# Optimization experiments

Hardware: AMD Instinct MI355X
Metric: run time of the kernel (lower is better)

## Reference

```python
import jax, jax.numpy as jnp
import numpy as np

N_NODES = 50000
N_EDGES = 600000
N_GRAPHS = 100
IN_DIM, HID, OUT = 128, 128, 64
K = 2  # DGL TAGConv default hop count


def setup_inputs() -> dict:
    key = jax.random.key(0)
    ks = jax.random.split(key, 8)
    x = jax.random.normal(ks[0], (N_NODES, IN_DIM), dtype=jnp.float32)
    src = jax.random.randint(ks[1], (N_EDGES,), 0, N_NODES)
    dst = jax.random.randint(ks[2], (N_EDGES,), 0, N_NODES)
    graph_id = jnp.sort(jax.random.randint(ks[3], (N_NODES,), 0, N_GRAPHS))
    # TAGConv lin: Linear(in_feats*(K+1), out_feats), stored as (in*(K+1), out)
    W1 = jax.random.normal(ks[4], (IN_DIM * (K + 1), HID), dtype=jnp.float32) / np.sqrt(IN_DIM * (K + 1))
    b1 = jnp.zeros((HID,), dtype=jnp.float32)
    W2 = jax.random.normal(ks[5], (HID * (K + 1), OUT), dtype=jnp.float32) / np.sqrt(HID * (K + 1))
    b2 = jnp.zeros((OUT,), dtype=jnp.float32)
    return {"x": x, "W1": W1, "b1": b1, "W2": W2, "b2": b2,
            "src": src, "dst": dst, "graph_id": graph_id}


def _tagconv(h, src, dst, norm, W, b):
    """DGL TAGConv: relu(concat_k (D^-1/2 A D^-1/2)^k h @ W + b), k=0..K."""
    feats = [h]
    cur = h
    for _ in range(K):
        cur = cur * norm[:, None]
        cur = jax.ops.segment_sum(cur[src], dst, num_segments=N_NODES)
        cur = cur * norm[:, None]
        feats.append(cur)
    out = jnp.concatenate(feats, axis=-1) @ W + b
    return jax.nn.relu(out)


def reference(x, W1, b1, W2, b2, src, dst, graph_id):
    # symmetric norm from in-degrees (clamped to 1), as in DGL TAGConv
    deg = jax.ops.segment_sum(jnp.ones_like(dst, dtype=x.dtype), dst, num_segments=N_NODES)
    norm = jnp.clip(deg, 1.0, None) ** -0.5
    h = _tagconv(x, src, dst, norm, W1, b1)
    h = _tagconv(h, src, dst, norm, W2, b2)
    # MaxPooling readout: per-graph max over nodes
    return jax.ops.segment_max(h, graph_id, num_segments=N_GRAPHS)
```

## Files before the change

### kernel.cpp

```cpp
#include <hip/hip_runtime.h>
#include <hip/hip_bf16.h>

#define N_NODES 50000
#define N_EDGES 600000
#define N_GRAPHS 100
#define M_PAD 50176

typedef __bf16 bf16_t;
typedef __attribute__((ext_vector_type(8))) __bf16 bf16x8;
typedef __attribute__((ext_vector_type(2))) __bf16 bf16x2;
typedef __attribute__((ext_vector_type(4))) float f32x4;

__global__ void degk(const int* __restrict__ dst, int* __restrict__ deg, int n) {
    int i = blockIdx.x * 256 + threadIdx.x;
    if (i < n) atomicAdd(&deg[dst[i]], 1);
}

__global__ void normk(const int* __restrict__ deg, float* __restrict__ norm, int n) {
    int i = blockIdx.x * 256 + threadIdx.x;
    if (i < n) {
        float d = fmaxf((float)deg[i], 1.0f);
        norm[i] = 1.0f / sqrtf(d);
    }
}

__global__ __launch_bounds__(1024) void scan1(const int* __restrict__ deg,
                                              int* __restrict__ row_off,
                                              int* __restrict__ partial, int n) {
    __shared__ int buf[1024];
    int i = blockIdx.x * 1024 + threadIdx.x;
    int v = (i < n) ? deg[i] : 0;
    buf[threadIdx.x] = v;
    __syncthreads();
    for (int off = 1; off < 1024; off <<= 1) {
        int t = (threadIdx.x >= off) ? buf[threadIdx.x - off] : 0;
        __syncthreads();
        buf[threadIdx.x] += t;
        __syncthreads();
    }
    if (i < n) row_off[i + 1] = buf[threadIdx.x];
    if (threadIdx.x == 1023) partial[blockIdx.x] = buf[1023];
}

__global__ void scan2(int* __restrict__ partial, int nchunks) {
    int lane = threadIdx.x;
    int v = (lane < nchunks) ? partial[lane] : 0;
    for (int off = 1; off < 64; off <<= 1) {
        int t = __shfl_up(v, off, 64);
        if (lane >= off) v += t;
    }
    int ex = __shfl_up(v, 1, 64);
    if (lane == 0) ex = 0;
    if (lane < nchunks) partial[lane] = ex;
}

__global__ void scan3(int* __restrict__ row_off, const int* __restrict__ partial, int n) {
    int i = blockIdx.x * 256 + threadIdx.x;
    if (i == 0) row_off[0] = 0;
    if (i < n) row_off[i + 1] += partial[i >> 10];
}

__global__ void scatterk(const int* __restrict__ src, const int* __restrict__ dst,
                         const int* __restrict__ row_off, int* __restrict__ cursor,
                         int* __restrict__ csr_src, int n) {
    int e = blockIdx.x * 256 + threadIdx.x;
    if (e >= n) return;
    int d = dst[e];
    int pos = atomicAdd(&cursor[d], 1);
    csr_src[row_off[d] + pos] = src[e];
}

__global__ void prescale(const float* __restrict__ x, const float* __restrict__ norm,
                         bf16_t* __restrict__ xb, bf16_t* __restrict__ xs, int n) {
    int i = blockIdx.x * 256 + threadIdx.x;
    if (i >= n * 64) return;
    int node = i >> 6;
    int c = (i & 63) * 2;
    float2 v = *(const float2*)(x + (size_t)node * 128 + c);
    float nd = norm[node];
    bf16x2 vb; vb[0] = (bf16_t)v.x; vb[1] = (bf16_t)v.y;
    bf16x2 vs; vs[0] = (bf16_t)(v.x * nd); vs[1] = (bf16_t)(v.y * nd);
    *(bf16x2*)(xb + (size_t)node * 128 + c) = vb;
    *(bf16x2*)(xs + (size_t)node * 128 + c) = vs;
}

__global__ void permW(const float* __restrict__ W, bf16_t* __restrict__ Wp, int K, int N) {
    int i = blockIdx.x * 256 + threadIdx.x;
    if (i >= K * N) return;
    int k = i / N, n = i - k * N;
    int kt = k >> 5, q = (k >> 3) & 3, j = k & 7;
    int nt = n >> 4, ln = n & 15;
    int lane = q * 16 + ln;
    Wp[(((size_t)kt * (N >> 4) + nt) * 64 + lane) * 8 + j] = (bf16_t)W[i];
}

template <bool SCALED>
__global__ __launch_bounds__(256) void spmm_bf16(const bf16_t* __restrict__ in,
                                                 bf16_t* __restrict__ out_c,
                                                 bf16_t* __restrict__ out_s,
                                                 const float* __restrict__ norm,
                                                 const int* __restrict__ row_off,
                                                 const int* __restrict__ csr_src, int n) {
    int tid = threadIdx.x;
    int sub = tid >> 4;
    int l   = tid & 15;
    int node = blockIdx.x * 16 + sub;
    if (node >= n) return;
    int e0 = row_off[node], e1 = row_off[node + 1];
    const bf16_t* col = in + l * 8;
    float acc[8] = {};
    int e = e0;
    for (; e + 4 <= e1; e += 4) {
        int s0 = csr_src[e + 0];
        int s1 = csr_src[e + 1];
        int s2 = csr_src[e + 2];
        int s3 = csr_src[e + 3];
        bf16x8 v0 = *(const bf16x8*)(col + (size_t)s0 * 128);
        bf16x8 v1 = *(const bf16x8*)(col + (size_t)s1 * 128);
        bf16x8 v2 = *(const bf16x8*)(col + (size_t)s2 * 128);
        bf16x8 v3 = *(const bf16x8*)(col + (size_t)s3 * 128);
#pragma unroll
        for (int j = 0; j < 8; j++)
            acc[j] += ((float)v0[j] + (float)v1[j]) + ((float)v2[j] + (float)v3[j]);
    }
    for (; e < e1; e++) {
        int s = csr_src[e];
        bf16x8 v = *(const bf16x8*)(col + (size_t)s * 128);
#pragma unroll
        for (int j = 0; j < 8; j++) acc[j] += (float)v[j];
    }
    float nd = norm[node];
    bf16x8 oc, os;
#pragma unroll
    for (int j = 0; j < 8; j++) {
        float c = acc[j] * nd;
        oc[j] = (bf16_t)c;
        os[j] = (bf16_t)(c * nd);
    }
    *(bf16x8*)(out_c + (size_t)node * 128 + l * 8) = oc;
    if (SCALED) *(bf16x8*)(out_s + (size_t)node * 128 + l * 8) = os;
}

template <int NT, bool LAYER1>
__global__ __launch_bounds__(256) void gemm_mfma(const bf16_t* __restrict__ f0,
                                                 const bf16_t* __restrict__ f1,
                                                 const bf16_t* __restrict__ f2,
                                                 const bf16_t* __restrict__ Wp,
                                                 const float* __restrict__ bias,
                                                 const float* __restrict__ norm,
                                                 bf16_t* __restrict__ out_b,
                                                 bf16_t* __restrict__ out_s,
                                                 float* __restrict__ out_f, int M) {
    int wave = threadIdx.x >> 6;
    int lane = threadIdx.x & 63;
    int q = lane >> 4, ln = lane & 15;
    int row0 = blockIdx.x * 128 + wave * 32;

    f32x4 acc[2][NT] = {};
    const bf16_t* feats[3] = {f0, f1, f2};
    const bf16x8* Wf = (const bf16x8*)Wp;

#pragma unroll
    for (int kc = 0; kc < 12; kc++) {
        const bf16_t* A = feats[kc >> 2] + (size_t)(kc & 3) * 32 + q * 8;
        bf16x8 a0 = *(const bf16x8*)(A + (size_t)(row0 + ln) * 128);
        bf16x8 a1 = *(const bf16x8*)(A + (size_t)(row0 + 16 + ln) * 128);
        const bf16x8* Bp = Wf + (size_t)kc * NT * 64 + lane;
#pragma unroll
        for (int nt = 0; nt < NT; nt++) {
            bf16x8 b = Bp[nt * 64];
            acc[0][nt] = __builtin_amdgcn_mfma_f32_16x16x32_bf16(a0, b, acc[0][nt], 0, 0, 0);
            acc[1][nt] = __builtin_amdgcn_mfma_f32_16x16x32_bf16(a1, b, acc[1][nt], 0, 0, 0);
        }
    }

    float bv[NT];
#pragma unroll
    for (int nt = 0; nt < NT; nt++) bv[nt] = bias[nt * 16 + ln];

#pragma unroll
    for (int mt = 0; mt < 2; mt++) {
#pragma unroll
        for (int r = 0; r < 4; r++) {
            int row = row0 + mt * 16 + q * 4 + r;
            if (row >= M) continue;
            float nd = LAYER1 ? norm[row] : 0.f;
#pragma unroll
            for (int nt = 0; nt < NT; nt++) {
                int col = nt * 16 + ln;
                float val = fmaxf(acc[mt][nt][r] + bv[nt], 0.f);
                if (LAYER1) {
                    out_b[(size_t)row * 128 + col] = (bf16_t)val;
                    out_s[(size_t)row * 128 + col] = (bf16_t)(val * nd);
                } else {
                    out_f[(size_t)row * 64 + col] = val;
                }
            }
        }
    }
}

__global__ __launch_bounds__(256) void maxpool2(const float* __restrict__ hF,
                                                const int* __restrict__ gid,
                                                unsigned int* __restrict__ out, int n) {
    int wave = threadIdx.x >> 6;
    int lane = threadIdx.x & 63;
    int n0 = blockIdx.x * 256 + wave * 64;
    if (n0 >= n) return;
    int n1 = min(n0 + 64, n);
    int cur = gid[n0];
    float m = 0.f;
    int i = n0;
    for (; i + 4 <= n1; i += 4) {
        int g0 = gid[i + 0], g1 = gid[i + 1], g2 = gid[i + 2], g3 = gid[i + 3];
        float v0 = hF[(size_t)(i + 0) * 64 + lane];
        float v1 = hF[(size_t)(i + 1) * 64 + lane];
        float v2 = hF[(size_t)(i + 2) * 64 + lane];
        float v3 = hF[(size_t)(i + 3) * 64 + lane];
        if (g0 != cur) { atomicMax(&out[cur * 64 + lane], __float_as_uint(m)); cur = g0; m = v0; } else m = fmaxf(m, v0);
        if (g1 != cur) { atomicMax(&out[cur * 64 + lane], __float_as_uint(m)); cur = g1; m = v1; } else m = fmaxf(m, v1);
        if (g2 != cur) { atomicMax(&out[cur * 64 + lane], __float_as_uint(m)); cur = g2; m = v2; } else m = fmaxf(m, v2);
        if (g3 != cur) { atomicMax(&out[cur * 64 + lane], __float_as_uint(m)); cur = g3; m = v3; } else m = fmaxf(m, v3);
    }
    for (; i < n1; i++) {
        int g = gid[i];
        float v = hF[(size_t)i * 64 + lane];
        if (g != cur) { atomicMax(&out[cur * 64 + lane], __float_as_uint(m)); cur = g; m = v; }
        else m = fmaxf(m, v);
    }
    atomicMax(&out[cur * 64 + lane], __float_as_uint(m));
}

extern "C" void kernel_launch(void* const* d_in, const int* in_sizes, int n_in,
                              void* d_out, int out_size, void* d_ws, size_t ws_size,
                              hipStream_t stream) {
    const float* x  = (const float*)d_in[0];
    const float* W1 = (const float*)d_in[1];
    const float* b1 = (const float*)d_in[2];
    const float* W2 = (const float*)d_in[3];
    const float* b2 = (const float*)d_in[4];
    const int* src  = (const int*)d_in[5];
    const int* dst  = (const int*)d_in[6];
    const int* gid  = (const int*)d_in[7];
    float* out = (float*)d_out;

    char* ws = (char*)d_ws;
    size_t off = 0;
    auto take = [&](size_t bytes) {
        void* p = ws + off;
        off = (off + bytes + 255) & ~(size_t)255;
        return p;
    };
    int* deg     = (int*)take((size_t)N_NODES * 4);
    int* cursor  = (int*)take((size_t)N_NODES * 4);
    size_t zero_bytes = off;
    float* norm  = (float*)take((size_t)N_NODES * 4);
    int* row_off = (int*)take((size_t)(N_NODES + 1) * 4);
    int* partial = (int*)take(64 * 4);
    int* csr_src = (int*)take((size_t)N_EDGES * 4);
    bf16_t* Wp1  = (bf16_t*)take((size_t)384 * 128 * 2);
    bf16_t* Wp2  = (bf16_t*)take((size_t)384 * 64 * 2);
    bf16_t* B0 = (bf16_t*)take((size_t)M_PAD * 128 * 2);
    bf16_t* B1 = (bf16_t*)take((size_t)M_PAD * 128 * 2);
    bf16_t* B2 = (bf16_t*)take((size_t)M_PAD * 128 * 2);
    bf16_t* B3 = (bf16_t*)take((size_t)M_PAD * 128 * 2);
    bf16_t* B4 = (bf16_t*)take((size_t)M_PAD * 128 * 2);
    bf16_t* B5 = (bf16_t*)take((size_t)M_PAD * 128 * 2);
    (void)ws_size; (void)in_sizes; (void)n_in; (void)out_size;

    hipMemsetAsync(d_ws, 0, zero_bytes, stream);
    hipMemsetAsync(d_out, 0, (size_t)N_GRAPHS * 64 * 4, stream);

    degk<<<(N_EDGES + 255) / 256, 256, 0, stream>>>(dst, deg, N_EDGES);
    normk<<<(N_NODES + 255) / 256, 256, 0, stream>>>(deg, norm, N_NODES);

    int nchunks = (N_NODES + 1023) / 1024;
    scan1<<<nchunks, 1024, 0, stream>>>(deg, row_off, partial, N_NODES);
    scan2<<<1, 64, 0, stream>>>(partial, nchunks);
    scan3<<<(N_NODES + 255) / 256, 256, 0, stream>>>(row_off, partial, N_NODES);
    scatterk<<<(N_EDGES + 255) / 256, 256, 0, stream>>>(src, dst, row_off, cursor, csr_src, N_EDGES);

    prescale<<<(N_NODES * 64 + 255) / 256, 256, 0, stream>>>(x, norm, B0, B1, N_NODES);
    permW<<<(384 * 128 + 255) / 256, 256, 0, stream>>>(W1, Wp1, 384, 128);
    permW<<<(384 * 64 + 255) / 256, 256, 0, stream>>>(W2, Wp2, 384, 64);

    int spmm_grid = (N_NODES + 15) / 16;
    int gemm_grid = M_PAD / 128;
    spmm_bf16<true><<<spmm_grid, 256, 0, stream>>>(B1, B2, B4, norm, row_off, csr_src, N_NODES);
    spmm_bf16<false><<<spmm_grid, 256, 0, stream>>>(B4, B3, nullptr, norm, row_off, csr_src, N_NODES);
    gemm_mfma<8, true><<<gemm_grid, 256, 0, stream>>>(B0, B2, B3, Wp1, b1, norm, B5, B1, nullptr, N_NODES);
    spmm_bf16<true><<<spmm_grid, 256, 0, stream>>>(B1, B2, B4, norm, row_off, csr_src, N_NODES);
    spmm_bf16<false><<<spmm_grid, 256, 0, stream>>>(B4, B3, nullptr, norm, row_off, csr_src, N_NODES);
    gemm_mfma<4, false><<<gemm_grid, 256, 0, stream>>>(B5, B2, B3, Wp2, b2, nullptr, nullptr, nullptr, (float*)B0, N_NODES);
    maxpool2<<<(N_NODES + 255) / 256, 256, 0, stream>>>((const float*)B0, gid, (unsigned int*)out, N_NODES);
}
```

Before: 308.8 us.

## Sort nodes by degree and process two nodes per SpMM thread group

Adds a counting sort of nodes by in-degree (histogram, scan, permutation) so neighbouring thread groups in the SpMM handle nodes with similar degree, which reduces wave divergence. Each 16-lane group now processes two nodes at once, interleaving their gathers so more loads are in flight. The cost is three extra small kernels, scattered output writes through the permutation, and higher register pressure from two accumulator sets.

```diff
diff --git a/kernel.cpp b/kernel.cpp
--- a/kernel.cpp
+++ b/kernel.cpp
@@ -70,6 +70,33 @@
     csr_src[row_off[d] + pos] = src[e];
 }
 
+__global__ void histk(const int* __restrict__ deg, int* __restrict__ hist, int n) {
+    int i = blockIdx.x * 256 + threadIdx.x;
+    if (i < n) atomicAdd(&hist[min(deg[i], 127)], 1);
+}
+
+__global__ void hscan(const int* __restrict__ hist, int* __restrict__ boff) {
+    __shared__ int b[128];
+    int t = threadIdx.x;
+    b[t] = hist[t];
+    __syncthreads();
+    if (t == 0) {
+        int s = 0;
+        for (int i = 0; i < 128; i++) { int v = b[i]; b[i] = s; s += v; }
+    }
+    __syncthreads();
+    boff[t] = b[t];
+}
+
+__global__ void permk(const int* __restrict__ deg, const int* __restrict__ boff,
+                      int* __restrict__ cur, int* __restrict__ perm, int n) {
+    int i = blockIdx.x * 256 + threadIdx.x;
+    if (i >= n) return;
+    int b = min(deg[i], 127);
+    int p = atomicAdd(&cur[b], 1);
+    perm[boff[b] + p] = i;
+}
+
 __global__ void prescale(const float* __restrict__ x, const float* __restrict__ norm,
                          bf16_t* __restrict__ xb, bf16_t* __restrict__ xs, int n) {
     int i = blockIdx.x * 256 + threadIdx.x;
@@ -100,45 +127,91 @@
                                                  bf16_t* __restrict__ out_s,
                                                  const float* __restrict__ norm,
                                                  const int* __restrict__ row_off,
-                                                 const int* __restrict__ csr_src, int n) {
+                                                 const int* __restrict__ csr_src,
+                                                 const int* __restrict__ perm, int n) {
     int tid = threadIdx.x;
     int sub = tid >> 4;
     int l   = tid & 15;
-    int node = blockIdx.x * 16 + sub;
-    if (node >= n) return;
-    int e0 = row_off[node], e1 = row_off[node + 1];
+    int base = blockIdx.x * 32 + sub * 2;
+    if (base >= n) return;
+    int nodeA = perm[base];
+    bool hasB = (base + 1 < n);
+    int nodeB = hasB ? perm[base + 1] : nodeA;
+
+    int a0 = row_off[nodeA], a1 = row_off[nodeA + 1];
+    int b0 = row_off[nodeB], b1 = row_off[nodeB + 1];
     const bf16_t* col = in + l * 8;
-    float acc[8] = {};
-    int e = e0;
-    for (; e + 4 <= e1; e += 4) {
-        int s0 = csr_src[e + 0];
-        int s1 = csr_src[e + 1];
-        int s2 = csr_src[e + 2];
-        int s3 = csr_src[e + 3];
+    float accA[8] = {}, accB[8] = {};
+
+    int da = a1 - a0, db = b1 - b0;
+    int c4 = (da < db ? da : db) & ~3;
+    int ea = a0, eb = b0;
+    for (int k = 0; k < c4; k += 4) {
+        int sA0 = csr_src[ea + 0], sA1 = csr_src[ea + 1], sA2 = csr_src[ea + 2], sA3 = csr_src[ea + 3];
+        int sB0 = csr_src[eb + 0], sB1 = csr_src[eb + 1], sB2 = csr_src[eb + 2], sB3 = csr_src[eb + 3];
+        bf16x8 vA0 = *(const bf16x8*)(col + (size_t)sA0 * 128);
+        bf16x8 vA1 = *(const bf16x8*)(col + (size_t)sA1 * 128);
+        bf16x8 vA2 = *(const bf16x8*)(col + (size_t)sA2 * 128);
+        bf16x8 vA3 = *(const bf16x8*)(col + (size_t)sA3 * 128);
+        bf16x8 vB0 = *(const bf16x8*)(col + (size_t)sB0 * 128);
+        bf16x8 vB1 = *(const bf16x8*)(col + (size_t)sB1 * 128);
+        bf16x8 vB2 = *(const bf16x8*)(col + (size_t)sB2 * 128);
+        bf16x8 vB3 = *(const bf16x8*)(col + (size_t)sB3 * 128);
+#pragma unroll
+        for (int j = 0; j < 8; j++) {
+            accA[j] += ((float)vA0[j] + (float)vA1[j]) + ((float)vA2[j] + (float)vA3[j]);
+            accB[j] += ((float)vB0[j] + (float)vB1[j]) + ((float)vB2[j] + (float)vB3[j]);
+        }
+        ea += 4; eb += 4;
+    }
+    for (; ea + 4 <= a1; ea += 4) {
+        int s0 = csr_src[ea + 0], s1 = csr_src[ea + 1], s2 = csr_src[ea + 2], s3 = csr_src[ea + 3];
         bf16x8 v0 = *(const bf16x8*)(col + (size_t)s0 * 128);
         bf16x8 v1 = *(const bf16x8*)(col + (size_t)s1 * 128);
         bf16x8 v2 = *(const bf16x8*)(col + (size_t)s2 * 128);
         bf16x8 v3 = *(const bf16x8*)(col + (size_t)s3 * 128);
 #pragma unroll
         for (int j = 0; j < 8; j++)
-            acc[j] += ((float)v0[j] + (float)v1[j]) + ((float)v2[j] + (float)v3[j]);
-    }
-    for (; e < e1; e++) {
-        int s = csr_src[e];
+            accA[j] += ((float)v0[j] + (float)v1[j]) + ((float)v2[j] + (float)v3[j]);
+    }
+    for (; ea < a1; ea++) {
+        int s = csr_src[ea];
         bf16x8 v = *(const bf16x8*)(col + (size_t)s * 128);
 #pragma unroll
-        for (int j = 0; j < 8; j++) acc[j] += (float)v[j];
-    }
-    float nd = norm[node];
-    bf16x8 oc, os;
+        for (int j = 0; j < 8; j++) accA[j] += (float)v[j];
+    }
+    for (; eb + 4 <= b1; eb += 4) {
+        int s0 = csr_src[eb + 0], s1 = csr_src[eb + 1], s2 = csr_src[eb + 2], s3 = csr_src[eb + 3];
+        bf16x8 v0 = *(const bf16x8*)(col + (size_t)s0 * 128);
+        bf16x8 v1 = *(const bf16x8*)(col + (size_t)s1 * 128);
+        bf16x8 v2 = *(const bf16x8*)(col + (size_t)s2 * 128);
+        bf16x8 v3 = *(const bf16x8*)(col + (size_t)s3 * 128);
+#pragma unroll
+        for (int j = 0; j < 8; j++)
+            accB[j] += ((float)v0[j] + (float)v1[j]) + ((float)v2[j] + (float)v3[j]);
+    }
+    for (; eb < b1; eb++) {
+        int s = csr_src[eb];
+        bf16x8 v = *(const bf16x8*)(col + (size_t)s * 128);
+#pragma unroll
+        for (int j = 0; j < 8; j++) accB[j] += (float)v[j];
+    }
+
+    float ndA = norm[nodeA], ndB = norm[nodeB];
+    bf16x8 ocA, osA, ocB, osB;
 #pragma unroll
     for (int j = 0; j < 8; j++) {
-        float c = acc[j] * nd;
-        oc[j] = (bf16_t)c;
-        os[j] = (bf16_t)(c * nd);
-    }
-    *(bf16x8*)(out_c + (size_t)node * 128 + l * 8) = oc;
-    if (SCALED) *(bf16x8*)(out_s + (size_t)node * 128 + l * 8) = os;
+        float cA = accA[j] * ndA;
+        ocA[j] = (bf16_t)cA; osA[j] = (bf16_t)(cA * ndA);
+        float cB = accB[j] * ndB;
+        ocB[j] = (bf16_t)cB; osB[j] = (bf16_t)(cB * ndB);
+    }
+    *(bf16x8*)(out_c + (size_t)nodeA * 128 + l * 8) = ocA;
+    if (SCALED) *(bf16x8*)(out_s + (size_t)nodeA * 128 + l * 8) = osA;
+    if (hasB) {
+        *(bf16x8*)(out_c + (size_t)nodeB * 128 + l * 8) = ocB;
+        if (SCALED) *(bf16x8*)(out_s + (size_t)nodeB * 128 + l * 8) = osB;
+    }
 }
 
 template <int NT, bool LAYER1>
@@ -253,10 +326,14 @@
     };
     int* deg     = (int*)take((size_t)N_NODES * 4);
     int* cursor  = (int*)take((size_t)N_NODES * 4);
+    int* hist    = (int*)take(128 * 4);
+    int* hcur    = (int*)take(128 * 4);
     size_t zero_bytes = off;
     float* norm  = (float*)take((size_t)N_NODES * 4);
     int* row_off = (int*)take((size_t)(N_NODES + 1) * 4);
     int* partial = (int*)take(64 * 4);
+    int* boff    = (int*)take(128 * 4);
+    int* perm    = (int*)take((size_t)N_NODES * 4);
     int* csr_src = (int*)take((size_t)N_EDGES * 4);
     bf16_t* Wp1  = (bf16_t*)take((size_t)384 * 128 * 2);
     bf16_t* Wp2  = (bf16_t*)take((size_t)384 * 64 * 2);
@@ -280,17 +357,21 @@
     scan3<<<(N_NODES + 255) / 256, 256, 0, stream>>>(row_off, partial, N_NODES);
     scatterk<<<(N_EDGES + 255) / 256, 256, 0, stream>>>(src, dst, row_off, cursor, csr_src, N_EDGES);
 
+    histk<<<(N_NODES + 255) / 256, 256, 0, stream>>>(deg, hist, N_NODES);
+    hscan<<<1, 128, 0, stream>>>(hist, boff);
+    permk<<<(N_NODES + 255) / 256, 256, 0, stream>>>(deg, boff, hcur, perm, N_NODES);
+
     prescale<<<(N_NODES * 64 + 255) / 256, 256, 0, stream>>>(x, norm, B0, B1, N_NODES);
     permW<<<(384 * 128 + 255) / 256, 256, 0, stream>>>(W1, Wp1, 384, 128);
     permW<<<(384 * 64 + 255) / 256, 256, 0, stream>>>(W2, Wp2, 384, 64);
 
-    int spmm_grid = (N_NODES + 15) / 16;
+    int spmm_grid = (N_NODES + 31) / 32;
     int gemm_grid = M_PAD / 128;
-    spmm_bf16<true><<<spmm_grid, 256, 0, stream>>>(B1, B2, B4, norm, row_off, csr_src, N_NODES);
-    spmm_bf16<false><<<spmm_grid, 256, 0, stream>>>(B4, B3, nullptr, norm, row_off, csr_src, N_NODES);
+    spmm_bf16<true><<<spmm_grid, 256, 0, stream>>>(B1, B2, B4, norm, row_off, csr_src, perm, N_NODES);
+    spmm_bf16<false><<<spmm_grid, 256, 0, stream>>>(B4, B3, nullptr, norm, row_off, csr_src, perm, N_NODES);
     gemm_mfma<8, true><<<gemm_grid, 256, 0, stream>>>(B0, B2, B3, Wp1, b1, norm, B5, B1, nullptr, N_NODES);
-    spmm_bf16<true><<<spmm_grid, 256, 0, stream>>>(B1, B2, B4, norm, row_off, csr_src, N_NODES);
-    spmm_bf16<false><<<spmm_grid, 256, 0, stream>>>(B4, B3, nullptr, norm, row_off, csr_src, N_NODES);
+    spmm_bf16<true><<<spmm_grid, 256, 0, stream>>>(B1, B2, B4, norm, row_off, csr_src, perm, N_NODES);
+    spmm_bf16<false><<<spmm_grid, 256, 0, stream>>>(B4, B3, nullptr, norm, row_off, csr_src, perm, N_NODES);
     gemm_mfma<4, false><<<gemm_grid, 256, 0, stream>>>(B5, B2, B3, Wp2, b2, nullptr, nullptr, nullptr, (float*)B0, N_NODES);
     maxpool2<<<(N_NODES + 255) / 256, 256, 0, stream>>>((const float*)B0, gid, (unsigned int*)out, N_NODES);
 }
```

Measured after the change: 642.2 us. +108.0%, slower.

## Split SpMM feature columns across blocks and stream CSR indices nontemporally

Applied to the files above, without the earlier changes.

The SpMM kernel is restructured so each block handles one 32-column slice of the 128-wide bf16 features for 64 nodes, with 4 threads per node instead of 16. Consecutive blocks take different column groups of the same node chunk. The aim is a smaller working set of gathered source rows per wave, which should improve cache locality, and the edge indices are loaded with nontemporal hints so they pollute the cache less. In exchange, each edge index and row offset is now read four times, and each gather moves only 64 bytes per row, which may waste memory transactions.

```diff
diff --git a/kernel.cpp b/kernel.cpp
--- a/kernel.cpp
+++ b/kernel.cpp
@@ -95,37 +95,39 @@
 }
 
 template <bool SCALED>
-__global__ __launch_bounds__(256) void spmm_bf16(const bf16_t* __restrict__ in,
-                                                 bf16_t* __restrict__ out_c,
-                                                 bf16_t* __restrict__ out_s,
-                                                 const float* __restrict__ norm,
-                                                 const int* __restrict__ row_off,
-                                                 const int* __restrict__ csr_src, int n) {
-    int tid = threadIdx.x;
-    int sub = tid >> 4;
-    int l   = tid & 15;
-    int node = blockIdx.x * 16 + sub;
+__global__ __launch_bounds__(256) void spmm_cb(const bf16_t* __restrict__ in,
+                                               bf16_t* __restrict__ out_c,
+                                               bf16_t* __restrict__ out_s,
+                                               const float* __restrict__ norm,
+                                               const int* __restrict__ row_off,
+                                               const int* __restrict__ csr_src, int n) {
+    int cg    = blockIdx.x & 3;
+    int chunk = blockIdx.x >> 2;
+    int sub = threadIdx.x >> 2;
+    int l   = threadIdx.x & 3;
+    int node = chunk * 64 + sub;
     if (node >= n) return;
+    int col = cg * 32 + l * 8;
+    const bf16_t* colp = in + col;
     int e0 = row_off[node], e1 = row_off[node + 1];
-    const bf16_t* col = in + l * 8;
     float acc[8] = {};
     int e = e0;
     for (; e + 4 <= e1; e += 4) {
-        int s0 = csr_src[e + 0];
-        int s1 = csr_src[e + 1];
-        int s2 = csr_src[e + 2];
-        int s3 = csr_src[e + 3];
-        bf16x8 v0 = *(const bf16x8*)(col + (size_t)s0 * 128);
-        bf16x8 v1 = *(const bf16x8*)(col + (size_t)s1 * 128);
-        bf16x8 v2 = *(const bf16x8*)(col + (size_t)s2 * 128);
-        bf16x8 v3 = *(const bf16x8*)(col + (size_t)s3 * 128);
+        int s0 = __builtin_nontemporal_load(csr_src + e + 0);
+        int s1 = __builtin_nontemporal_load(csr_src + e + 1);
+        int s2 = __builtin_nontemporal_load(csr_src + e + 2);
+        int s3 = __builtin_nontemporal_load(csr_src + e + 3);
+        bf16x8 v0 = *(const bf16x8*)(colp + (size_t)s0 * 128);
+        bf16x8 v1 = *(const bf16x8*)(colp + (size_t)s1 * 128);
+        bf16x8 v2 = *(const bf16x8*)(colp + (size_t)s2 * 128);
+        bf16x8 v3 = *(const bf16x8*)(colp + (size_t)s3 * 128);
 #pragma unroll
         for (int j = 0; j < 8; j++)
             acc[j] += ((float)v0[j] + (float)v1[j]) + ((float)v2[j] + (float)v3[j]);
     }
     for (; e < e1; e++) {
-        int s = csr_src[e];
-        bf16x8 v = *(const bf16x8*)(col + (size_t)s * 128);
+        int s = __builtin_nontemporal_load(csr_src + e);
+        bf16x8 v = *(const bf16x8*)(colp + (size_t)s * 128);
 #pragma unroll
         for (int j = 0; j < 8; j++) acc[j] += (float)v[j];
     }
@@ -137,8 +139,8 @@
         oc[j] = (bf16_t)c;
         os[j] = (bf16_t)(c * nd);
     }
-    *(bf16x8*)(out_c + (size_t)node * 128 + l * 8) = oc;
-    if (SCALED) *(bf16x8*)(out_s + (size_t)node * 128 + l * 8) = os;
+    *(bf16x8*)(out_c + (size_t)node * 128 + col) = oc;
+    if (SCALED) *(bf16x8*)(out_s + (size_t)node * 128 + col) = os;
 }
 
 template <int NT, bool LAYER1>
@@ -284,13 +286,13 @@
     permW<<<(384 * 128 + 255) / 256, 256, 0, stream>>>(W1, Wp1, 384, 128);
     permW<<<(384 * 64 + 255) / 256, 256, 0, stream>>>(W2, Wp2, 384, 64);
 
-    int spmm_grid = (N_NODES + 15) / 16;
+    int spmm_grid = ((N_NODES + 63) / 64) * 4;
     int gemm_grid = M_PAD / 128;
-    spmm_bf16<true><<<spmm_grid, 256, 0, stream>>>(B1, B2, B4, norm, row_off, csr_src, N_NODES);
-    spmm_bf16<false><<<spmm_grid, 256, 0, stream>>>(B4, B3, nullptr, norm, row_off, csr_src, N_NODES);
+    spmm_cb<true><<<spmm_grid, 256, 0, stream>>>(B1, B2, B4, norm, row_off, csr_src, N_NODES);
+    spmm_cb<false><<<spmm_grid, 256, 0, stream>>>(B4, B3, nullptr, norm, row_off, csr_src, N_NODES);
     gemm_mfma<8, true><<<gemm_grid, 256, 0, stream>>>(B0, B2, B3, Wp1, b1, norm, B5, B1, nullptr, N_NODES);
-    spmm_bf16<true><<<spmm_grid, 256, 0, stream>>>(B1, B2, B4, norm, row_off, csr_src, N_NODES);
-    spmm_bf16<false><<<spmm_grid, 256, 0, stream>>>(B4, B3, nullptr, norm, row_off, csr_src, N_NODES);
+    spmm_cb<true><<<spmm_grid, 256, 0, stream>>>(B1, B2, B4, norm, row_off, csr_src, N_NODES);
+    spmm_cb<false><<<spmm_grid, 256, 0, stream>>>(B4, B3, nullptr, norm, row_off, csr_src, N_NODES);
     gemm_mfma<4, false><<<gemm_grid, 256, 0, stream>>>(B5, B2, B3, Wp2, b2, nullptr, nullptr, nullptr, (float*)B0, N_NODES);
     maxpool2<<<(N_NODES + 255) / 256, 256, 0, stream>>>((const float*)B0, gid, (unsigned int*)out, N_NODES);
 }
```

After: 380.0 us. +23.1%, slower.
